# Optimization experiments

Measured on AMD Instinct MI355X. Metric: run time of the kernel, lower is better.

## Reference

```python
import jax, jax.numpy as jnp
import numpy as np

B = 4096
D_IN = 1024
H1 = 2048
H2 = 1024
E = 7          # num_experts, forced by broadcasting in source
T = 2          # num_tasks
NS = 7         # scene dimension of S
EMB_ROWS = 10
EMB_DIM = 16


def setup_inputs() -> dict:
    key = jax.random.key(0)
    ks = jax.random.split(key, 8)
    x = jax.random.normal(ks[0], (B, D_IN), dtype=jnp.float32)
    scene = jax.random.randint(ks[1], (B,), 0, E)
    # Expert MLP params, stacked over experts: Linear(D_IN->H1)+ReLU, Linear(H1->H2)+ReLU
    W1 = jax.random.normal(ks[2], (E, D_IN, H1), dtype=jnp.float32) * (1.0 / np.sqrt(D_IN))
    b1 = jnp.zeros((E, H1), dtype=jnp.float32)
    W2 = jax.random.normal(ks[3], (E, H1, H2), dtype=jnp.float32) * (1.0 / np.sqrt(H1))
    b2 = jnp.zeros((E, H2), dtype=jnp.float32)
    # Routing tensor S: [7, input_dim+16, num_experts] (xavier-like init)
    S = jax.random.normal(ks[4], (NS, D_IN + EMB_DIM, E), dtype=jnp.float32) * 0.02
    scene_emb = jax.random.normal(ks[5], (EMB_ROWS, EMB_DIM), dtype=jnp.float32)
    return {"x": x, "scene": scene, "W1": W1, "b1": b1, "W2": W2, "b2": b2,
            "S": S, "scene_emb": scene_emb}


def _forward(x, scene, W1, b1, W2, b2, S, scene_emb):
    # Experts (vectorized over the E expert MLPs): [B,E,H2]
    h = jax.nn.relu(jnp.einsum('bd,edh->beh', x, W1) + b1)
    experts_out = jax.nn.relu(jnp.einsum('beh,eho->beo', h, W2) + b2)

    se = scene_emb[scene]                       # [B,16]
    xc = jnp.concatenate([x, se], axis=-1)      # [B, D_IN+16]
    G = jnp.einsum('bd,sde->bse', xc, S)        # [B, 7, E]
    G = jnp.transpose(G, (0, 2, 1))             # [B, E, 7]
    G = jax.nn.softmax(G, axis=-1)

    logG = jnp.log(G)                           # [B, E, 7]
    q = jnp.sum(jnp.log(G * 7.0) / 7.0, axis=-1)  # [B, E]

    KG = jnp.eye(E, dtype=x.dtype)
    ses = KG[scene][:, None, :]                 # [B, 1, E]

    _, pi = jax.lax.top_k(jnp.sum(ses * logG, axis=-1), 6)  # [B,6]
    _, qi = jax.lax.top_k(q, 6)                              # [B,6]
    select = ((KG[pi].sum(axis=1) + KG[qi].sum(axis=1)) > 0).astype(x.dtype)  # [B,E]

    gate = jax.nn.softmax(jnp.sum(G * ses, axis=-1), axis=-1) * select  # [B,E]
    out = jnp.einsum('be,bed->bd', gate, experts_out)                    # [B,H2]
    # self.gate ModuleList is unused in the source forward; each task output is identical
    return jnp.stack([out] * T, axis=0)         # [T, B, H2]


def reference(x, scene, W1, b1, W2, b2, S, scene_emb):
    return _forward(x, scene, W1, b1, W2, b2, S, scene_emb)
```

## Files before the change

kernel.cpp:

```cpp
#include <hip/hip_runtime.h>
#include <hip/hip_bf16.h>

typedef unsigned short u16;
typedef __bf16 bf8 __attribute__((ext_vector_type(8)));
typedef float f4 __attribute__((ext_vector_type(4)));

__device__ __forceinline__ u16 f2bf(float f) {
    unsigned int u = __float_as_uint(f);
    u = (u + 0x7fffu + ((u >> 16) & 1u)) >> 16;
    return (u16)u;
}

__device__ __forceinline__ void gload16(const u16* g, u16* l) {
    __builtin_amdgcn_global_load_lds((const __attribute__((address_space(1))) void*)g,
                                     (__attribute__((address_space(3))) void*)l, 16, 0, 0);
}

__global__ void transpose_cvt_kernel(const float* __restrict__ in, u16* __restrict__ out,
                                     int R, int C) {
    __shared__ u16 t[64][71];
    int e = blockIdx.z;
    int c0 = blockIdx.x * 64, r0 = blockIdx.y * 64;
    int tid = threadIdx.x;
    const float* ip = in + (size_t)e * R * C;
    u16* op = out + (size_t)e * R * C;
#pragma unroll
    for (int k = 0; k < 16; ++k) {
        int idx = k * 256 + tid;
        int r = idx >> 6, c = idx & 63;
        t[c][r] = f2bf(ip[(size_t)(r0 + r) * C + c0 + c]);
    }
    __syncthreads();
#pragma unroll
    for (int k = 0; k < 8; ++k) {
        int c = k * 8 + (tid >> 5);
        int rr = (tid & 31) * 2;
        ushort2 v = make_ushort2(t[c][rr], t[c][rr + 1]);
        *(ushort2*)(op + (size_t)(c0 + c) * R + r0 + rr) = v;
    }
}

__global__ void transpose_S_kernel(const float* __restrict__ S, float* __restrict__ ST) {
    int idx = blockIdx.x * 256 + threadIdx.x;
    if (idx >= 1040 * 52) return;
    int d = idx / 52, c = idx % 52;
    ST[idx] = (c < 49) ? S[(c / 7) * 7280 + d * 7 + (c % 7)] : 0.f;
}

__global__ void gating_kernel(const float* __restrict__ x, const int* __restrict__ scene,
                              const float* __restrict__ ST, const float* __restrict__ semb,
                              float* __restrict__ gate, u16* __restrict__ xb) {
    __shared__ float xc[4][1040];
    __shared__ float Lsh[4][49];
    int wv = threadIdx.x >> 6, lane = threadIdx.x & 63;
    int row = blockIdx.x * 4 + wv;
    float* xcw = xc[wv];
    const float* xr = x + (size_t)row * 1024;
    for (int d = lane; d < 1024; d += 64) xcw[d] = xr[d];
    int sc = scene[row];
    if (lane < 16) xcw[1024 + lane] = semb[sc * 16 + lane];
    __syncthreads();

    u16* xrow = xb + (size_t)row * 1024;
    for (int d = lane * 4; d < 1024; d += 256) {
        ushort4 o;
        o.x = f2bf(xcw[d]);     o.y = f2bf(xcw[d + 1]);
        o.z = f2bf(xcw[d + 2]); o.w = f2bf(xcw[d + 3]);
        *(ushort4*)(xrow + d) = o;
    }

    if (lane < 49) {
        const float* STp = ST + lane;
        float a0 = 0.f, a1 = 0.f, a2 = 0.f, a3 = 0.f;
        for (int d = 0; d < 1040; d += 4) {
            a0 += xcw[d]     * STp[d * 52];
            a1 += xcw[d + 1] * STp[d * 52 + 52];
            a2 += xcw[d + 2] * STp[d * 52 + 104];
            a3 += xcw[d + 3] * STp[d * 52 + 156];
        }
        Lsh[wv][lane] = (a0 + a1) + (a2 + a3);
    }
    __syncthreads();

    if (lane == 0) {
        float logG[7][7], Gsc[7], piS[7], qS[7];
        for (int e = 0; e < 7; e++) {
            float L[7];
            float m = -1e30f;
            for (int s = 0; s < 7; s++) { L[s] = Lsh[wv][s * 7 + e]; m = fmaxf(m, L[s]); }
            float sum = 0.f;
            for (int s = 0; s < 7; s++) sum += expf(L[s] - m);
            float lse = m + logf(sum);
            float qs = 0.f;
            for (int s = 0; s < 7; s++) { logG[e][s] = L[s] - lse; qs += logG[e][s]; }
            piS[e] = logG[e][sc];
            qS[e] = qs;
            Gsc[e] = expf(logG[e][sc]);
        }
        int epi = 0, eqi = 0; float bp = piS[0], bq = qS[0];
        for (int e = 1; e < 7; e++) {
            if (piS[e] <= bp) { bp = piS[e]; epi = e; }
            if (qS[e]  <= bq) { bq = qS[e];  eqi = e; }
        }
        float mg = -1e30f;
        for (int e = 0; e < 7; e++) mg = fmaxf(mg, Gsc[e]);
        float sum = 0.f;
        float ex[7];
        for (int e = 0; e < 7; e++) { ex[e] = expf(Gsc[e] - mg); sum += ex[e]; }
        float inv = 1.f / sum;
        for (int e = 0; e < 7; e++) {
            float g = ex[e] * inv;
            if (e == epi && e == eqi) g = 0.f;
            gate[row * 7 + e] = g;
        }
    }
}

template<bool G2>
__global__ __launch_bounds__(512, 2) void gemm8p_kernel(
    const u16* __restrict__ Abase, const u16* __restrict__ Bbase,
    const float* __restrict__ bias, const float* __restrict__ gate,
    void* __restrict__ outp, float* __restrict__ part, int* __restrict__ flags)
{
    constexpr int M = 4096;
    constexpr int K = G2 ? 2048 : 1024;
    constexpr int N = G2 ? 1024 : 2048;
    constexpr int NT = K / 64;
    constexpr int LOG2NT = G2 ? 5 : 4;

    extern __shared__ u16 lds[];

    const int tid = threadIdx.x;
    const int lane = tid & 63;
    const int wid = tid >> 6;
    const int wr = wid >> 2, wc = wid & 3;
    const int ln15 = lane & 15, lnk = (lane >> 4) * 8;

    int bm, bn, e0, nE, grp;
    if constexpr (G2) {
        int id = blockIdx.x;
        int xcd = id & 7, slot = id >> 3;
        grp = xcd & 1;
        bn = slot & 3;
        bm = (slot >> 2) * 4 + (xcd >> 1);
        e0 = grp ? 3 : 0; nE = grp ? 4 : 3;
    } else {
        int xcd = blockIdx.x & 7, slot = blockIdx.x >> 3;
        bn = slot >> 2;
        bm = (slot & 3) * 8 + xcd;
        e0 = 0; nE = 7; grp = 0;
    }
    const int NTtot = nE * NT;

    const int sr = tid >> 3;
    const int sc = (tid & 7) * 8;

    auto stageA = [&](int gt, int buf) {
#pragma unroll
        for (int l = 0; l < 2; ++l) {
            int r = l * 64 + sr;
            int cs = sc ^ ((r & 7) << 3);
            const u16* g = Abase + (G2 ? (size_t)(e0 + (gt >> LOG2NT)) * M * K : (size_t)0)
                         + (size_t)(bm * 128 + r) * K + (gt & (NT - 1)) * 64 + cs;
            gload16(g, lds + buf * 24576 + l * 4096 + tid * 8);
        }
    };
    auto stageB = [&](int gt, int buf, int h) {
#pragma unroll
        for (int l = 0; l < 2; ++l) {
            int rb = h * 128 + l * 64 + sr;
            int cs = sc ^ ((rb & 7) << 3);
            const u16* g = Bbase + (size_t)(e0 + (gt >> LOG2NT)) * N * K
                         + (size_t)(bn * 256 + rb) * K + (gt & (NT - 1)) * 64 + cs;
            gload16(g, lds + buf * 24576 + 8192 + h * 8192 + l * 4096 + tid * 8);
        }
    };
    auto aoff = [&](int mi, int ks) {
        int r = wr * 64 + mi * 16 + ln15;
        int c = ks * 32 + lnk;
        return r * 64 + (c ^ ((r & 7) << 3));
    };
    auto boff = [&](int ni, int ks) {
        int rb = wc * 64 + ni * 16 + ln15;
        int c = ks * 32 + lnk;
        return rb * 64 + (c ^ ((rb & 7) << 3));
    };

    f4 acc[4][4] = {};
    f4 fin[4][4] = {};
    bf8 aA[2][2], bL[2][2], bH[2][2];

    stageA(0, 0); stageB(0, 0, 0); stageB(0, 0, 1);

    for (int gt = 0; gt < NTtot; ++gt) {
        const int cur = gt & 1, nxt = cur ^ 1;
        const bool more = (gt + 1 < NTtot);
        const u16* Ac = lds + cur * 24576;
        const u16* Bc = lds + cur * 24576 + 8192;
        if (more) {
            stageA(gt + 1, nxt); stageB(gt + 1, nxt, 0);
            asm volatile("s_waitcnt vmcnt(4)" ::: "memory");
        } else {
            asm volatile("s_waitcnt vmcnt(0)" ::: "memory");
        }
        __builtin_amdgcn_sched_barrier(0);
        __builtin_amdgcn_s_barrier();
        __builtin_amdgcn_sched_barrier(0);
#pragma unroll
        for (int mi = 0; mi < 2; ++mi)
#pragma unroll
            for (int ks = 0; ks < 2; ++ks)
                aA[mi][ks] = *(const bf8*)(Ac + aoff(mi, ks));
#pragma unroll
        for (int ni = 0; ni < 2; ++ni)
#pragma unroll
            for (int ks = 0; ks < 2; ++ks)
                bL[ni][ks] = *(const bf8*)(Bc + boff(ni, ks));
        asm volatile("s_waitcnt lgkmcnt(0)" ::: "memory");
        __builtin_amdgcn_sched_barrier(0);
        __builtin_amdgcn_s_setprio(1);
#pragma unroll
        for (int mi = 0; mi < 2; ++mi)
#pragma unroll
            for (int ni = 0; ni < 2; ++ni)
#pragma unroll
                for (int ks = 0; ks < 2; ++ks)
                    acc[mi][ni] = __builtin_amdgcn_mfma_f32_16x16x32_bf16(aA[mi][ks], bL[ni][ks], acc[mi][ni], 0, 0, 0);
        __builtin_amdgcn_s_setprio(0);
        if (more) stageB(gt + 1, nxt, 1);
#pragma unroll
        for (int ni = 0; ni < 2; ++ni)
#pragma unroll
            for (int ks = 0; ks < 2; ++ks)
                bH[ni][ks] = *(const bf8*)(Bc + boff(2 + ni, ks));
        asm volatile("s_waitcnt lgkmcnt(0)" ::: "memory");
        __builtin_amdgcn_sched_barrier(0);
        __builtin_amdgcn_s_setprio(1);
#pragma unroll
        for (int mi = 0; mi < 2; ++mi)
#pragma unroll
            for (int ni = 0; ni < 2; ++ni)
#pragma unroll
                for (int ks = 0; ks < 2; ++ks)
                    acc[mi][2 + ni] = __builtin_amdgcn_mfma_f32_16x16x32_bf16(aA[mi][ks], bH[ni][ks], acc[mi][2 + ni], 0, 0, 0);
        __builtin_amdgcn_s_setprio(0);
#pragma unroll
        for (int mi = 0; mi < 2; ++mi)
#pragma unroll
            for (int ks = 0; ks < 2; ++ks)
                aA[mi][ks] = *(const bf8*)(Ac + aoff(2 + mi, ks));
        asm volatile("s_waitcnt lgkmcnt(0)" ::: "memory");
        __builtin_amdgcn_sched_barrier(0);
        __builtin_amdgcn_s_setprio(1);
#pragma unroll
        for (int mi = 0; mi < 2; ++mi)
#pragma unroll
            for (int ni = 0; ni < 2; ++ni)
#pragma unroll
                for (int ks = 0; ks < 2; ++ks)
                    acc[2 + mi][2 + ni] = __builtin_amdgcn_mfma_f32_16x16x32_bf16(aA[mi][ks], bH[ni][ks], acc[2 + mi][2 + ni], 0, 0, 0);
        __builtin_amdgcn_s_setprio(0);
        __builtin_amdgcn_sched_barrier(0);
        __builtin_amdgcn_s_barrier();
        __builtin_amdgcn_sched_barrier(0);
        __builtin_amdgcn_s_setprio(1);
#pragma unroll
        for (int mi = 0; mi < 2; ++mi)
#pragma unroll
            for (int ni = 0; ni < 2; ++ni)
#pragma unroll
                for (int ks = 0; ks < 2; ++ks)
                    acc[2 + mi][ni] = __builtin_amdgcn_mfma_f32_16x16x32_bf16(aA[mi][ks], bL[ni][ks], acc[2 + mi][ni], 0, 0, 0);
        __builtin_amdgcn_s_setprio(0);
        __builtin_amdgcn_sched_barrier(0);
        if ((gt & (NT - 1)) == NT - 1) {
            int e = e0 + (gt >> LOG2NT);
            float bloc[4];
#pragma unroll
            for (int ni = 0; ni < 4; ++ni)
                bloc[ni] = bias[e * N + bn * 256 + wc * 64 + ni * 16 + ln15];
            if constexpr (G2) {
#pragma unroll
                for (int mi = 0; mi < 4; ++mi)
#pragma unroll
                    for (int i = 0; i < 4; ++i) {
                        int row = bm * 128 + wr * 64 + mi * 16 + (lane >> 4) * 4 + i;
                        float g = gate[row * 7 + e];
#pragma unroll
                        for (int ni = 0; ni < 4; ++ni) {
                            fin[mi][ni][i] += g * fmaxf(acc[mi][ni][i] + bloc[ni], 0.f);
                            acc[mi][ni][i] = 0.f;
                        }
                    }
            } else {
                u16* Hp = (u16*)outp + (size_t)e * M * N;
#pragma unroll
                for (int mi = 0; mi < 4; ++mi)
#pragma unroll
                    for (int i = 0; i < 4; ++i) {
                        size_t row = (size_t)(bm * 128 + wr * 64 + mi * 16 + (lane >> 4) * 4 + i);
#pragma unroll
                        for (int ni = 0; ni < 4; ++ni) {
                            __builtin_nontemporal_store(
                                f2bf(fmaxf(acc[mi][ni][i] + bloc[ni], 0.f)),
                                &Hp[row * N + bn * 256 + wc * 64 + ni * 16 + ln15]);
                            acc[mi][ni][i] = 0.f;
                        }
                    }
            }
        }
    }

    if constexpr (G2) {
        const int fi = bm * 4 + bn;
        if (grp == 0) {
#pragma unroll
            for (int mi = 0; mi < 4; ++mi)
#pragma unroll
                for (int i = 0; i < 4; ++i) {
                    size_t row = (size_t)(bm * 128 + wr * 64 + mi * 16 + (lane >> 4) * 4 + i);
#pragma unroll
                    for (int ni = 0; ni < 4; ++ni)
                        __hip_atomic_store(&part[row * N + bn * 256 + wc * 64 + ni * 16 + ln15],
                                           fin[mi][ni][i],
                                           __ATOMIC_RELAXED, __HIP_MEMORY_SCOPE_AGENT);
                }
            __syncthreads();
            if (tid == 0)
                __hip_atomic_store(&flags[fi], 1, __ATOMIC_RELEASE, __HIP_MEMORY_SCOPE_AGENT);
        } else {
            if (tid == 0) {
                while (__hip_atomic_load(&flags[fi], __ATOMIC_ACQUIRE, __HIP_MEMORY_SCOPE_AGENT) == 0)
                    __builtin_amdgcn_s_sleep(8);
            }
            __syncthreads();
            float* out0 = (float*)outp;
#pragma unroll
            for (int mi = 0; mi < 4; ++mi)
#pragma unroll
                for (int i = 0; i < 4; ++i) {
                    size_t row = (size_t)(bm * 128 + wr * 64 + mi * 16 + (lane >> 4) * 4 + i);
#pragma unroll
                    for (int ni = 0; ni < 4; ++ni) {
                        size_t idx = row * N + bn * 256 + wc * 64 + ni * 16 + ln15;
                        float v = fin[mi][ni][i] +
                                  __hip_atomic_load(&part[idx], __ATOMIC_RELAXED,
                                                    __HIP_MEMORY_SCOPE_AGENT);
                        out0[idx] = v;
                        out0[(size_t)M * N + idx] = v;
                    }
                }
        }
    }
}

extern "C" void kernel_launch(void* const* d_in, const int* in_sizes, int n_in,
                              void* d_out, int out_size, void* d_ws, size_t ws_size,
                              hipStream_t stream) {
    const float* x     = (const float*)d_in[0];
    const int*   scene = (const int*)d_in[1];
    const float* W1    = (const float*)d_in[2];
    const float* b1    = (const float*)d_in[3];
    const float* W2    = (const float*)d_in[4];
    const float* b2    = (const float*)d_in[5];
    const float* S     = (const float*)d_in[6];
    const float* semb  = (const float*)d_in[7];
    float* out = (float*)d_out;

    char* ws = (char*)d_ws;
    float* part  = (float*)(ws);
    u16*   xb    = (u16*)(ws);
    u16*   W1T   = (u16*)(ws + 8388608);
    int*   flags = (int*)(ws + 16777216 + 20971520);
    u16*   W2T   = (u16*)(ws + 37748736);
    u16*   Hb    = (u16*)(ws + 67108864);
    float* gate  = (float*)(ws + 184549376);
    float* ST    = (float*)(ws + 184664064);
    flags        = (int*)(ws + 16777216);

    (void)hipFuncSetAttribute(reinterpret_cast<const void*>(gemm8p_kernel<false>),
                              hipFuncAttributeMaxDynamicSharedMemorySize, 98304);
    (void)hipFuncSetAttribute(reinterpret_cast<const void*>(gemm8p_kernel<true>),
                              hipFuncAttributeMaxDynamicSharedMemorySize, 98304);

    transpose_cvt_kernel<<<dim3(32, 16, 7), 256, 0, stream>>>(W1, W1T, 1024, 2048);
    transpose_cvt_kernel<<<dim3(16, 32, 7), 256, 0, stream>>>(W2, W2T, 2048, 1024);
    transpose_S_kernel<<<(1040 * 52 + 255) / 256, 256, 0, stream>>>(S, ST);
    gating_kernel<<<1024, 256, 0, stream>>>(x, scene, ST, semb, gate, xb);
    gemm8p_kernel<false><<<256, 512, 98304, stream>>>(xb, W1T, b1, nullptr, Hb, nullptr, nullptr);
    (void)hipMemsetAsync(flags, 0, 512, stream);
    gemm8p_kernel<true><<<256, 512, 98304, stream>>>(Hb, W2T, b2, gate, out, part, flags);
}
```

Baseline: 358.4 us.

## Balance second GEMM by splitting expert 3 K-range across the two block groups

The second GEMM previously gave one block group three experts (96 K-tiles) and the other four (128 K-tiles). Now expert 3 is split: group 0 does its first 8 K-tiles and publishes the partial sum, and group 1 does the remaining 24 tiles. Group 1 then adds the partial, applies bias, ReLU and gate, and combines with group 0's result. The per-block load becomes 104 vs 120 tiles instead of 96 vs 128. This adds an extra partial buffer, a second flag handshake and one more spin-wait.

```diff
diff --git a/kernel.cpp b/kernel.cpp
--- a/kernel.cpp
+++ b/kernel.cpp
@@ -120,13 +120,12 @@
 __global__ __launch_bounds__(512, 2) void gemm8p_kernel(
     const u16* __restrict__ Abase, const u16* __restrict__ Bbase,
     const float* __restrict__ bias, const float* __restrict__ gate,
-    void* __restrict__ outp, float* __restrict__ part, int* __restrict__ flags)
+    void* __restrict__ outp, float* __restrict__ part3, float* __restrict__ partF,
+    int* __restrict__ flags)
 {
     constexpr int M = 4096;
     constexpr int K = G2 ? 2048 : 1024;
     constexpr int N = G2 ? 1024 : 2048;
-    constexpr int NT = K / 64;
-    constexpr int LOG2NT = G2 ? 5 : 4;
 
     extern __shared__ u16 lds[];
 
@@ -136,42 +135,56 @@
     const int wr = wid >> 2, wc = wid & 3;
     const int ln15 = lane & 15, lnk = (lane >> 4) * 8;
 
-    int bm, bn, e0, nE, grp;
+    int bm, bn, grp, NTtot;
     if constexpr (G2) {
         int id = blockIdx.x;
         int xcd = id & 7, slot = id >> 3;
         grp = xcd & 1;
         bn = slot & 3;
         bm = (slot >> 2) * 4 + (xcd >> 1);
-        e0 = grp ? 3 : 0; nE = grp ? 4 : 3;
+        NTtot = grp ? 120 : 104;
     } else {
         int xcd = blockIdx.x & 7, slot = blockIdx.x >> 3;
         bn = slot >> 2;
         bm = (slot & 3) * 8 + xcd;
-        e0 = 0; nE = 7; grp = 0;
-    }
-    const int NTtot = nE * NT;
+        grp = 0; NTtot = 112;
+    }
+    const int fi = G2 ? (bm * 4 + bn) : 0;
+
+    auto ekt = [&](int gt, int& e, int& kt) {
+        if constexpr (G2) {
+            if (grp == 0) {
+                if (gt < 8) { e = 3; kt = gt; }
+                else        { e = (gt - 8) >> 5; kt = (gt - 8) & 31; }
+            } else {
+                if (gt < 96) { e = 4 + (gt >> 5); kt = gt & 31; }
+                else         { e = 3; kt = gt - 88; }
+            }
+        } else { e = gt >> 4; kt = gt & 15; }
+    };
 
     const int sr = tid >> 3;
     const int sc = (tid & 7) * 8;
 
     auto stageA = [&](int gt, int buf) {
+        int e, kt; ekt(gt, e, kt);
 #pragma unroll
         for (int l = 0; l < 2; ++l) {
             int r = l * 64 + sr;
             int cs = sc ^ ((r & 7) << 3);
-            const u16* g = Abase + (G2 ? (size_t)(e0 + (gt >> LOG2NT)) * M * K : (size_t)0)
-                         + (size_t)(bm * 128 + r) * K + (gt & (NT - 1)) * 64 + cs;
+            const u16* g = Abase + (G2 ? (size_t)e * M * K : (size_t)0)
+                         + (size_t)(bm * 128 + r) * K + kt * 64 + cs;
             gload16(g, lds + buf * 24576 + l * 4096 + tid * 8);
         }
     };
     auto stageB = [&](int gt, int buf, int h) {
+        int e, kt; ekt(gt, e, kt);
 #pragma unroll
         for (int l = 0; l < 2; ++l) {
             int rb = h * 128 + l * 64 + sr;
             int cs = sc ^ ((rb & 7) << 3);
-            const u16* g = Bbase + (size_t)(e0 + (gt >> LOG2NT)) * N * K
-                         + (size_t)(bn * 256 + rb) * K + (gt & (NT - 1)) * 64 + cs;
+            const u16* g = Bbase + (size_t)e * N * K
+                         + (size_t)(bn * 256 + rb) * K + kt * 64 + cs;
             gload16(g, lds + buf * 24576 + 8192 + h * 8192 + l * 4096 + tid * 8);
         }
     };
@@ -273,26 +286,54 @@
                     acc[2 + mi][ni] = __builtin_amdgcn_mfma_f32_16x16x32_bf16(aA[mi][ks], bL[ni][ks], acc[2 + mi][ni], 0, 0, 0);
         __builtin_amdgcn_s_setprio(0);
         __builtin_amdgcn_sched_barrier(0);
-        if ((gt & (NT - 1)) == NT - 1) {
-            int e = e0 + (gt >> LOG2NT);
-            float bloc[4];
-#pragma unroll
-            for (int ni = 0; ni < 4; ++ni)
-                bloc[ni] = bias[e * N + bn * 256 + wc * 64 + ni * 16 + ln15];
+        bool bnd;
+        if constexpr (G2) bnd = (grp == 0) ? (gt == 7 || gt == 39 || gt == 71 || gt == 103)
+                                           : (gt == 31 || gt == 63 || gt == 95);
+        else bnd = ((gt & 15) == 15);
+        if (bnd) {
             if constexpr (G2) {
-#pragma unroll
-                for (int mi = 0; mi < 4; ++mi)
-#pragma unroll
-                    for (int i = 0; i < 4; ++i) {
-                        int row = bm * 128 + wr * 64 + mi * 16 + (lane >> 4) * 4 + i;
-                        float g = gate[row * 7 + e];
-#pragma unroll
-                        for (int ni = 0; ni < 4; ++ni) {
-                            fin[mi][ni][i] += g * fmaxf(acc[mi][ni][i] + bloc[ni], 0.f);
-                            acc[mi][ni][i] = 0.f;
+                if (grp == 0 && gt == 7) {
+#pragma unroll
+                    for (int mi = 0; mi < 4; ++mi)
+#pragma unroll
+                        for (int i = 0; i < 4; ++i) {
+                            size_t row = (size_t)(bm * 128 + wr * 64 + mi * 16 + (lane >> 4) * 4 + i);
+#pragma unroll
+                            for (int ni = 0; ni < 4; ++ni) {
+                                __hip_atomic_store(&part3[row * N + bn * 256 + wc * 64 + ni * 16 + ln15],
+                                                   acc[mi][ni][i],
+                                                   __ATOMIC_RELAXED, __HIP_MEMORY_SCOPE_AGENT);
+                                acc[mi][ni][i] = 0.f;
+                            }
                         }
-                    }
+                    __syncthreads();
+                    if (tid == 0)
+                        __hip_atomic_store(&flags[fi], 1, __ATOMIC_RELEASE, __HIP_MEMORY_SCOPE_AGENT);
+                } else {
+                    int e = (grp == 0) ? ((gt - 8) >> 5) : (4 + (gt >> 5));
+                    float bloc[4];
+#pragma unroll
+                    for (int ni = 0; ni < 4; ++ni)
+                        bloc[ni] = bias[e * N + bn * 256 + wc * 64 + ni * 16 + ln15];
+#pragma unroll
+                    for (int mi = 0; mi < 4; ++mi)
+#pragma unroll
+                        for (int i = 0; i < 4; ++i) {
+                            int row = bm * 128 + wr * 64 + mi * 16 + (lane >> 4) * 4 + i;
+                            float g = gate[row * 7 + e];
+#pragma unroll
+                            for (int ni = 0; ni < 4; ++ni) {
+                                fin[mi][ni][i] += g * fmaxf(acc[mi][ni][i] + bloc[ni], 0.f);
+                                acc[mi][ni][i] = 0.f;
+                            }
+                        }
+                }
             } else {
+                int e = gt >> 4;
+                float bloc[4];
+#pragma unroll
+                for (int ni = 0; ni < 4; ++ni)
+                    bloc[ni] = bias[e * N + bn * 256 + wc * 64 + ni * 16 + ln15];
                 u16* Hp = (u16*)outp + (size_t)e * M * N;
 #pragma unroll
                 for (int mi = 0; mi < 4; ++mi)
@@ -312,7 +353,6 @@
     }
 
     if constexpr (G2) {
-        const int fi = bm * 4 + bn;
         if (grp == 0) {
 #pragma unroll
             for (int mi = 0; mi < 4; ++mi)
@@ -321,19 +361,44 @@
                     size_t row = (size_t)(bm * 128 + wr * 64 + mi * 16 + (lane >> 4) * 4 + i);
 #pragma unroll
                     for (int ni = 0; ni < 4; ++ni)
-                        __hip_atomic_store(&part[row * N + bn * 256 + wc * 64 + ni * 16 + ln15],
+                        __hip_atomic_store(&partF[row * N + bn * 256 + wc * 64 + ni * 16 + ln15],
                                            fin[mi][ni][i],
                                            __ATOMIC_RELAXED, __HIP_MEMORY_SCOPE_AGENT);
                 }
             __syncthreads();
             if (tid == 0)
-                __hip_atomic_store(&flags[fi], 1, __ATOMIC_RELEASE, __HIP_MEMORY_SCOPE_AGENT);
+                __hip_atomic_store(&flags[128 + fi], 1, __ATOMIC_RELEASE, __HIP_MEMORY_SCOPE_AGENT);
         } else {
             if (tid == 0) {
                 while (__hip_atomic_load(&flags[fi], __ATOMIC_ACQUIRE, __HIP_MEMORY_SCOPE_AGENT) == 0)
                     __builtin_amdgcn_s_sleep(8);
             }
             __syncthreads();
+            {
+                float bloc[4];
+#pragma unroll
+                for (int ni = 0; ni < 4; ++ni)
+                    bloc[ni] = bias[3 * N + bn * 256 + wc * 64 + ni * 16 + ln15];
+#pragma unroll
+                for (int mi = 0; mi < 4; ++mi)
+#pragma unroll
+                    for (int i = 0; i < 4; ++i) {
+                        int row = bm * 128 + wr * 64 + mi * 16 + (lane >> 4) * 4 + i;
+                        float g = gate[row * 7 + 3];
+#pragma unroll
+                        for (int ni = 0; ni < 4; ++ni) {
+                            size_t idx = (size_t)row * N + bn * 256 + wc * 64 + ni * 16 + ln15;
+                            float full3 = acc[mi][ni][i] +
+                                __hip_atomic_load(&part3[idx], __ATOMIC_RELAXED, __HIP_MEMORY_SCOPE_AGENT);
+                            fin[mi][ni][i] += g * fmaxf(full3 + bloc[ni], 0.f);
+                        }
+                    }
+            }
+            if (tid == 0) {
+                while (__hip_atomic_load(&flags[128 + fi], __ATOMIC_ACQUIRE, __HIP_MEMORY_SCOPE_AGENT) == 0)
+                    __builtin_amdgcn_s_sleep(8);
+            }
+            __syncthreads();
             float* out0 = (float*)outp;
 #pragma unroll
             for (int mi = 0; mi < 4; ++mi)
@@ -344,7 +409,7 @@
                     for (int ni = 0; ni < 4; ++ni) {
                         size_t idx = row * N + bn * 256 + wc * 64 + ni * 16 + ln15;
                         float v = fin[mi][ni][i] +
-                                  __hip_atomic_load(&part[idx], __ATOMIC_RELAXED,
+                                  __hip_atomic_load(&partF[idx], __ATOMIC_RELAXED,
                                                     __HIP_MEMORY_SCOPE_AGENT);
                         out0[idx] = v;
                         out0[(size_t)M * N + idx] = v;
@@ -368,15 +433,15 @@
     float* out = (float*)d_out;
 
     char* ws = (char*)d_ws;
-    float* part  = (float*)(ws);
+    float* part3 = (float*)(ws);
+    float* partF = (float*)(ws + 16777216);
+    int*   flags = (int*)(ws + 33554432);
     u16*   xb    = (u16*)(ws);
     u16*   W1T   = (u16*)(ws + 8388608);
-    int*   flags = (int*)(ws + 16777216 + 20971520);
     u16*   W2T   = (u16*)(ws + 37748736);
     u16*   Hb    = (u16*)(ws + 67108864);
     float* gate  = (float*)(ws + 184549376);
     float* ST    = (float*)(ws + 184664064);
-    flags        = (int*)(ws + 16777216);
 
     (void)hipFuncSetAttribute(reinterpret_cast<const void*>(gemm8p_kernel<false>),
                               hipFuncAttributeMaxDynamicSharedMemorySize, 98304);
@@ -387,7 +452,9 @@
     transpose_cvt_kernel<<<dim3(16, 32, 7), 256, 0, stream>>>(W2, W2T, 2048, 1024);
     transpose_S_kernel<<<(1040 * 52 + 255) / 256, 256, 0, stream>>>(S, ST);
     gating_kernel<<<1024, 256, 0, stream>>>(x, scene, ST, semb, gate, xb);
-    gemm8p_kernel<false><<<256, 512, 98304, stream>>>(xb, W1T, b1, nullptr, Hb, nullptr, nullptr);
-    (void)hipMemsetAsync(flags, 0, 512, stream);
-    gemm8p_kernel<true><<<256, 512, 98304, stream>>>(Hb, W2T, b2, gate, out, part, flags);
-}
+    gemm8p_kernel<false><<<256, 512, 98304, stream>>>(xb, W1T, b1, nullptr, Hb,
+                                                      nullptr, nullptr, nullptr);
+    (void)hipMemsetAsync(flags, 0, 2048, stream);
+    gemm8p_kernel<true><<<256, 512, 98304, stream>>>(Hb, W2T, b2, gate, out,
+                                                     part3, partF, flags);
+}
```

After: 391.2 us. +9.2%, slower.
